# Optimization experiments

Measured on AMD Instinct MI355X. Metric: run time of the kernel, lower is better.

The kernel has to match this reference:

```python
import jax, jax.numpy as jnp
import numpy as np

N_NODES = 100000
C = 128
E = 800000
V = 50000
NEG_SLOPE = 0.2


def gat_conv(x, edges, W, att_src, att_dst, bias, num_nodes):
    """Single-head PyG-style GATConv with self-loops added (PyG default).

    edges: [2, E] with row 0 = source j, row 1 = destination i.
    """
    loops = jnp.arange(num_nodes, dtype=edges.dtype)
    src = jnp.concatenate([edges[0], loops])  # [E+N]
    dst = jnp.concatenate([edges[1], loops])

    h = x @ W.T                               # [N, C] linear transform
    a_s = h @ att_src                         # [N] per-node src score
    a_d = h @ att_dst                         # [N] per-node dst score

    e = jax.nn.leaky_relu(a_s[src] + a_d[dst], NEG_SLOPE)  # [E+N]
    # scatter-softmax over edges grouped by destination node
    m = jax.ops.segment_max(e, dst, num_segments=num_nodes)
    ex = jnp.exp(e - m[dst])
    denom = jax.ops.segment_sum(ex, dst, num_segments=num_nodes)
    alpha = ex / (denom[dst] + 1e-16)         # [E+N]

    out = jax.ops.segment_sum(alpha[:, None] * h[src], dst, num_segments=num_nodes)
    return out + bias


def setup_inputs() -> dict:
    key = jax.random.key(0)
    ks = jax.random.split(key, 12)
    s = 1.0 / np.sqrt(C)
    return {
        "embedding": jax.random.normal(ks[0], (N_NODES, C), jnp.float32),
        "W1": jax.random.normal(ks[1], (C, C), jnp.float32) * s,
        "att_src1": jax.random.normal(ks[2], (C,), jnp.float32) * s,
        "att_dst1": jax.random.normal(ks[3], (C,), jnp.float32) * s,
        "b1": jax.random.normal(ks[4], (C,), jnp.float32) * s,
        "W2": jax.random.normal(ks[5], (C, C), jnp.float32) * s,
        "att_src2": jax.random.normal(ks[6], (C,), jnp.float32) * s,
        "att_dst2": jax.random.normal(ks[7], (C,), jnp.float32) * s,
        "b2": jax.random.normal(ks[8], (C,), jnp.float32) * s,
        "edges1": jax.random.randint(ks[9], (2, E), 0, N_NODES, jnp.int64 if jax.config.jax_enable_x64 else jnp.int32),
        "edges2": jax.random.randint(ks[10], (2, E), 0, N_NODES, jnp.int64 if jax.config.jax_enable_x64 else jnp.int32),
        "idx_mapping": jax.random.randint(ks[11], (V,), 0, N_NODES, jnp.int64 if jax.config.jax_enable_x64 else jnp.int32),
    }


def reference(embedding, W1, att_src1, att_dst1, b1, W2, att_src2, att_dst2, b2,
              edges1, edges2, idx_mapping):
    h = gat_conv(embedding, edges1, W1, att_src1, att_dst1, b1, N_NODES)
    h = gat_conv(h, edges2, W2, att_src2, att_dst2, b2, N_NODES)
    return h[idx_mapping]
```

## Files before the change

kernel.cpp:

```cpp
#include <hip/hip_runtime.h>

#define N_NODES 100000
#define C_DIM 128
#define E_EDGES 800000
#define V_OUT 50000
#define EN (E_EDGES + N_NODES)
#define M2 (2 * N_NODES)
#define EN2 (2 * EN)

#define BSHIFT 8
#define NBUCK_L ((N_NODES + 255) >> 8)
#define NBUCK2 (2 * NBUCK_L)
#define CAP 4096
#define P1_CHUNK 4096
#define P1_PER_T (P1_CHUNK / 256)
#define NCHUNK ((EN2 + P1_CHUNK - 1) / P1_CHUNK)
#define VFLAG_BLKS ((V_OUT + 255) / 256)

#define XPAD 136
#define LDS_E 768

#define GEMM_BLKS ((N_NODES + 63) / 64)

typedef unsigned int uint;
typedef unsigned short ushort;
typedef __attribute__((ext_vector_type(8))) short bf16x8;
typedef __attribute__((ext_vector_type(4))) float f32x4;

static __device__ __forceinline__ ushort f2bf(float f) {
    uint u = __float_as_uint(f);
    u += 0x7fffu + ((u >> 16) & 1);
    return (ushort)(u >> 16);
}

template <int IN_F32>
static __device__ __forceinline__ void gemm_body(
    char* smem, int gb, int tid,
    const void* __restrict__ xin, const float* __restrict__ W,
    const float* __restrict__ att_s, const float* __restrict__ att_d,
    ushort* __restrict__ hb, float* __restrict__ a_s, float* __restrict__ a_d)
{
    ushort* ws = (ushort*)smem;

    {
        const int row = tid >> 1, half = tid & 1;
        const float* src = W + row * 128 + half * 64;
        ushort* dst = &ws[row * XPAD + half * 64];
        #pragma unroll
        for (int i = 0; i < 8; ++i) {
            float4 u = *reinterpret_cast<const float4*>(src + i * 8);
            float4 v = *reinterpret_cast<const float4*>(src + i * 8 + 4);
            uint4 pk;
            pk.x = (uint)f2bf(u.x) | ((uint)f2bf(u.y) << 16);
            pk.y = (uint)f2bf(u.z) | ((uint)f2bf(u.w) << 16);
            pk.z = (uint)f2bf(v.x) | ((uint)f2bf(v.y) << 16);
            pk.w = (uint)f2bf(v.z) | ((uint)f2bf(v.w) << 16);
            *reinterpret_cast<uint4*>(dst + i * 8) = pk;
        }
    }

    const int lane = tid & 63, wv = tid >> 6;
    const int m = lane & 15, quad = lane >> 4;
    const int nb = gb * 64;
    const int n0 = nb + wv * 16;
    const long xrow = min((long)(n0 + m), (long)N_NODES - 1);

    bf16x8 a[4];
    if (IN_F32) {
        const float* src = (const float*)xin + xrow * 128 + quad * 8;
        #pragma unroll
        for (int ki = 0; ki < 4; ++ki) {
            float4 u = *reinterpret_cast<const float4*>(src + ki * 32);
            float4 v = *reinterpret_cast<const float4*>(src + ki * 32 + 4);
            uint4 pk;
            pk.x = (uint)f2bf(u.x) | ((uint)f2bf(u.y) << 16);
            pk.y = (uint)f2bf(u.z) | ((uint)f2bf(u.w) << 16);
            pk.z = (uint)f2bf(v.x) | ((uint)f2bf(v.y) << 16);
            pk.w = (uint)f2bf(v.z) | ((uint)f2bf(v.w) << 16);
            a[ki] = *reinterpret_cast<bf16x8*>(&pk);
        }
    } else {
        const ushort* src = (const ushort*)xin + xrow * 128 + quad * 8;
        #pragma unroll
        for (int ki = 0; ki < 4; ++ki)
            a[ki] = *reinterpret_cast<const bf16x8*>(src + ki * 32);
    }
    __syncthreads();

    float ps[4] = {0, 0, 0, 0}, pd[4] = {0, 0, 0, 0};
    uint2 packed[8];
    #pragma unroll
    for (int ct = 0; ct < 8; ++ct) {
        const int cc = ct * 16 + m;
        f32x4 acc = {0.f, 0.f, 0.f, 0.f};
        #pragma unroll
        for (int ki = 0; ki < 4; ++ki) {
            bf16x8 b = *reinterpret_cast<const bf16x8*>(&ws[cc * XPAD + quad * 8 + ki * 32]);
            acc = __builtin_amdgcn_mfma_f32_16x16x32_bf16(a[ki], b, acc, 0, 0, 0);
        }
        const float asc = att_s[cc], adc = att_d[cc];
        #pragma unroll
        for (int r = 0; r < 4; ++r) {
            ps[r] = fmaf(acc[r], asc, ps[r]);
            pd[r] = fmaf(acc[r], adc, pd[r]);
        }
        packed[ct].x = (uint)f2bf(acc[0]) | ((uint)f2bf(acc[1]) << 16);
        packed[ct].y = (uint)f2bf(acc[2]) | ((uint)f2bf(acc[3]) << 16);
    }
    __syncthreads();

    {
        const int rowb = (wv * 16 + quad * 4) * XPAD + m;
        #pragma unroll
        for (int ct = 0; ct < 8; ++ct) {
            ws[rowb            + ct * 16] = (ushort)(packed[ct].x);
            ws[rowb +     XPAD + ct * 16] = (ushort)(packed[ct].x >> 16);
            ws[rowb + 2 * XPAD + ct * 16] = (ushort)(packed[ct].y);
            ws[rowb + 3 * XPAD + ct * 16] = (ushort)(packed[ct].y >> 16);
        }
    }
    __syncthreads();

    {
        const int sub = tid & 15, rb = tid >> 4;
        #pragma unroll
        for (int i = 0; i < 4; ++i) {
            const int rl = rb + i * 16;
            const int node = nb + rl;
            uint4 v = *reinterpret_cast<const uint4*>(&ws[rl * XPAD + sub * 8]);
            if (node < N_NODES)
                *reinterpret_cast<uint4*>(hb + (long)node * 128 + sub * 8) = v;
        }
    }
    #pragma unroll
    for (int r = 0; r < 4; ++r) {
        float s = ps[r], d = pd[r];
        #pragma unroll
        for (int x = 1; x < 16; x <<= 1) { s += __shfl_xor(s, x); d += __shfl_xor(d, x); }
        const int node = n0 + quad * 4 + r;
        if (m == 0 && node < N_NODES) { a_s[node] = s; a_d[node] = d; }
    }
}

static __device__ __forceinline__ void partition_body(
    char* smem, int pb, int tid,
    const int* __restrict__ e1, const int* __restrict__ e2,
    int* __restrict__ cursor, uint* __restrict__ slab)
{
    int* cnt     = (int*)smem;
    int* basearr = cnt + NBUCK2;
    for (int i = tid; i < NBUCK2; i += 256) cnt[i] = 0;
    __syncthreads();

    const int e0 = pb * P1_CHUNK;
    uint ent[P1_PER_T];
    int  bkt[P1_PER_T];
    #pragma unroll
    for (int i = 0; i < P1_PER_T; ++i) {
        int e = e0 + i * 256 + tid;
        bkt[i] = -1;
        if (e < EN2) {
            int src, dst, lb;
            if (e < EN) {
                if (e < E_EDGES) { src = e1[e]; dst = e1[E_EDGES + e]; }
                else             { src = dst = e - E_EDGES; }
                lb = 0;
            } else {
                int f = e - EN;
                if (f < E_EDGES) { src = e2[f]; dst = e2[E_EDGES + f]; }
                else             { src = dst = f - E_EDGES; }
                lb = NBUCK_L;
            }
            bkt[i] = lb + (dst >> BSHIFT);
            ent[i] = (uint)src | ((uint)(dst & 255) << 17);
            atomicAdd(&cnt[bkt[i]], 1);
        }
    }
    __syncthreads();
    for (int b = tid; b < NBUCK2; b += 256) {
        int c = cnt[b];
        basearr[b] = (c > 0) ? atomicAdd(&cursor[b], c) : 0;
        cnt[b] = 0;
    }
    __syncthreads();
    #pragma unroll
    for (int i = 0; i < P1_PER_T; ++i) {
        if (bkt[i] >= 0) {
            int r = basearr[bkt[i]] + atomicAdd(&cnt[bkt[i]], 1);
            if (r < CAP) slab[(long)bkt[i] * CAP + r] = ent[i];
        }
    }
}

__global__ __launch_bounds__(256, 4) void front_kernel(
    const float* __restrict__ emb, const float* __restrict__ W1,
    const float* __restrict__ as1, const float* __restrict__ ad1,
    ushort* __restrict__ hb, float* __restrict__ aS, float* __restrict__ aD,
    const int* __restrict__ e1, const int* __restrict__ e2,
    int* __restrict__ cursor, uint* __restrict__ slab,
    const int* __restrict__ idxm, int* __restrict__ head, int* __restrict__ nextp)
{
    __shared__ __attribute__((aligned(16))) char smem[128 * XPAD * 2];
    const int b = blockIdx.x;
    const int tid = threadIdx.x;
    if (b < GEMM_BLKS) {
        gemm_body<1>(smem, b, tid, emb, W1, as1, ad1, hb, aS, aD);
    } else if (b < GEMM_BLKS + NCHUNK) {
        partition_body(smem, b - GEMM_BLKS, tid, e1, e2, cursor, slab);
    } else {
        int v = (b - GEMM_BLKS - NCHUNK) * 256 + tid;
        if (v < V_OUT) {
            int n = idxm[v];
            int old = atomicExch(&head[n], v + 1);
            nextp[v] = old;
        }
    }
}

__global__ __launch_bounds__(256, 4) void gemm2_kernel(
    const ushort* __restrict__ a1o, const float* __restrict__ W2,
    const float* __restrict__ as2, const float* __restrict__ ad2,
    ushort* __restrict__ hb, float* __restrict__ aS, float* __restrict__ aD)
{
    __shared__ __attribute__((aligned(16))) char smem[128 * XPAD * 2];
    gemm_body<0>(smem, blockIdx.x, threadIdx.x, a1o, W2, as2, ad2, hb, aS, aD);
}

__global__ __launch_bounds__(256) void local_csr(
    const uint* __restrict__ slab, const int* __restrict__ cursor,
    int* __restrict__ offs, uint* __restrict__ esrc)
{
    __shared__ uint ent[CAP];
    __shared__ int deg[256];
    __shared__ int excl[256];
    __shared__ int sbase;
    const int b = blockIdx.x;
    const int tid = threadIdx.x;
    const int cnt = min(cursor[b], CAP);
    const int layer = (b >= NBUCK_L);
    const int node0 = (b - layer * NBUCK_L) << BSHIFT;
    const int obase = layer * N_NODES;
    const int nodes_n = min(256, N_NODES - node0);

    if (tid < 256) deg[tid & 255] = 0;
    if (tid < 64) {
        int s = 0;
        #pragma unroll
        for (int k = 0; k < 13; ++k) {
            int idx = tid + 64 * k;
            if (idx < b) s += cursor[idx];
        }
        #pragma unroll
        for (int d = 32; d > 0; d >>= 1) s += __shfl_down(s, d);
        if (tid == 0) sbase = s;
    }
    __syncthreads();
    const int base = sbase;

    for (int i = tid; i < cnt; i += 256) {
        uint v = slab[(long)b * CAP + i];
        ent[i] = v;
        atomicAdd(&deg[v >> 17], 1);
    }
    __syncthreads();
    if (tid < 64) {
        int v4[4]; int s = 0;
        #pragma unroll
        for (int i = 0; i < 4; ++i) { v4[i] = deg[tid * 4 + i]; s += v4[i]; }
        int incl = s;
        #pragma unroll
        for (int d = 1; d < 64; d <<= 1) {
            int t = __shfl_up(incl, d);
            if (tid >= d) incl += t;
        }
        int e = incl - s;
        #pragma unroll
        for (int i = 0; i < 4; ++i) { excl[tid * 4 + i] = e; e += v4[i]; }
    }
    __syncthreads();
    for (int i = tid; i < nodes_n; i += 256)
        offs[obase + node0 + i] = base + excl[i];
    if (tid < 256) deg[tid & 255] = 0;
    if (tid == 0 && node0 + 256 >= N_NODES)
        offs[obase + N_NODES] = base + cnt;
    __syncthreads();
    for (int i = tid; i < cnt; i += 256) {
        uint v = ent[i];
        int dl = v >> 17;
        int r = atomicAdd(&deg[dl], 1);
        esrc[base + excl[dl] + r] = v;
    }
}

template <int MODE>
__global__ __launch_bounds__(256) void aggregate(
    const ushort* __restrict__ hb, const float* __restrict__ a_s,
    const float* __restrict__ a_d, const float* __restrict__ bias,
    const int* __restrict__ offs, const uint* __restrict__ esrc,
    const int* __restrict__ head, const int* __restrict__ nextp,
    void* __restrict__ outp, int obase)
{
    __shared__ uint2 ew[LDS_E];
    const int tid = threadIdx.x;
    const int node0 = blockIdx.x * 16;
    const int bnode0 = (node0 >> BSHIFT) << BSHIFT;
    const int bstart = offs[obase + node0];
    const int bend   = offs[obase + node0 + 16];
    const int nE = bend - bstart;

    for (int i = tid; i < min(nE, LDS_E); i += 256) {
        uint v = esrc[bstart + i];
        float w = 0.0f;
        const int d = bnode0 + (v >> 17);
        if (MODE == 0 || head[d] != 0) {
            float e = a_s[v & 0x1ffff] + a_d[d];
            e = (e >= 0.0f) ? e : 0.2f * e;
            w = __expf(e);
        }
        ew[i] = make_uint2(v, __float_as_uint(w));
    }
    __syncthreads();

    const int wave = tid >> 6;
    const int lane = tid & 63;
    const int slot = lane >> 4;
    const int c16  = lane & 15;
    const int node = node0 + wave * 4 + slot;
    int hv = 0;
    if (MODE == 1) {
        hv = head[node];
        if (hv == 0) return;
    }

    const int start = offs[obase + node];
    const int end   = offs[obase + node + 1];
    const long coff = (long)(c16 << 3);
    float acc[8] = {0, 0, 0, 0, 0, 0, 0, 0};
    float dsum = 0.0f;

    if (start < end) {
        if (nE <= LDS_E) {
            const int jr = start - bstart, jend = end - bstart;
            const int e1 = jend - 1;
            uint2 p0 = ew[jr];
            uint2 p1 = ew[min(jr + 1, e1)];
            uint2 p2 = ew[min(jr + 2, e1)];
            uint2 p3 = ew[min(jr + 3, e1)];
            uint4 h0 = *reinterpret_cast<const uint4*>(hb + ((long)(p0.x & 0x1ffff) << 7) + coff);
            uint4 h1 = *reinterpret_cast<const uint4*>(hb + ((long)(p1.x & 0x1ffff) << 7) + coff);
            uint4 h2 = *reinterpret_cast<const uint4*>(hb + ((long)(p2.x & 0x1ffff) << 7) + coff);
            uint4 h3 = *reinterpret_cast<const uint4*>(hb + ((long)(p3.x & 0x1ffff) << 7) + coff);
            float w0 = __uint_as_float(p0.y);
            float w1 = __uint_as_float(p1.y);
            float w2 = __uint_as_float(p2.y);
            float w3 = __uint_as_float(p3.y);
            for (int j = jr; j < jend; ++j) {
                uint2 p4 = ew[min(j + 4, e1)];
                uint4 h4 = *reinterpret_cast<const uint4*>(hb + ((long)(p4.x & 0x1ffff) << 7) + coff);
                float w4 = __uint_as_float(p4.y);
                dsum += w0;
                acc[0] = fmaf(w0, __uint_as_float(h0.x << 16),         acc[0]);
                acc[1] = fmaf(w0, __uint_as_float(h0.x & 0xffff0000u), acc[1]);
                acc[2] = fmaf(w0, __uint_as_float(h0.y << 16),         acc[2]);
                acc[3] = fmaf(w0, __uint_as_float(h0.y & 0xffff0000u), acc[3]);
                acc[4] = fmaf(w0, __uint_as_float(h0.z << 16),         acc[4]);
                acc[5] = fmaf(w0, __uint_as_float(h0.z & 0xffff0000u), acc[5]);
                acc[6] = fmaf(w0, __uint_as_float(h0.w << 16),         acc[6]);
                acc[7] = fmaf(w0, __uint_as_float(h0.w & 0xffff0000u), acc[7]);
                w0 = w1; w1 = w2; w2 = w3; w3 = w4;
                h0 = h1; h1 = h2; h2 = h3; h3 = h4;
            }
        } else {
            const float ad = a_d[node];
            for (int j = start; j < end; ++j) {
                uint v = esrc[j];
                float e = a_s[v & 0x1ffff] + ad;
                e = (e >= 0.0f) ? e : 0.2f * e;
                float w = __expf(e);
                uint4 h = *reinterpret_cast<const uint4*>(hb + ((long)(v & 0x1ffff) << 7) + coff);
                dsum += w;
                acc[0] = fmaf(w, __uint_as_float(h.x << 16),         acc[0]);
                acc[1] = fmaf(w, __uint_as_float(h.x & 0xffff0000u), acc[1]);
                acc[2] = fmaf(w, __uint_as_float(h.y << 16),         acc[2]);
                acc[3] = fmaf(w, __uint_as_float(h.y & 0xffff0000u), acc[3]);
                acc[4] = fmaf(w, __uint_as_float(h.z << 16),         acc[4]);
                acc[5] = fmaf(w, __uint_as_float(h.z & 0xffff0000u), acc[5]);
                acc[6] = fmaf(w, __uint_as_float(h.w << 16),         acc[6]);
                acc[7] = fmaf(w, __uint_as_float(h.w & 0xffff0000u), acc[7]);
            }
        }
    }

    const float inv = 1.0f / (dsum + 1e-16f);
    const int c0 = c16 << 3;
    const float4 b0 = *reinterpret_cast<const float4*>(bias + c0);
    const float4 b1 = *reinterpret_cast<const float4*>(bias + c0 + 4);
    float res[8];
    res[0] = fmaf(acc[0], inv, b0.x);
    res[1] = fmaf(acc[1], inv, b0.y);
    res[2] = fmaf(acc[2], inv, b0.z);
    res[3] = fmaf(acc[3], inv, b0.w);
    res[4] = fmaf(acc[4], inv, b1.x);
    res[5] = fmaf(acc[5], inv, b1.y);
    res[6] = fmaf(acc[6], inv, b1.z);
    res[7] = fmaf(acc[7], inv, b1.w);
    if (MODE == 0) {
        uint4 pk;
        pk.x = (uint)f2bf(res[0]) | ((uint)f2bf(res[1]) << 16);
        pk.y = (uint)f2bf(res[2]) | ((uint)f2bf(res[3]) << 16);
        pk.z = (uint)f2bf(res[4]) | ((uint)f2bf(res[5]) << 16);
        pk.w = (uint)f2bf(res[6]) | ((uint)f2bf(res[7]) << 16);
        *reinterpret_cast<uint4*>((ushort*)outp + ((long)node << 7) + c0) = pk;
    } else {
        const float4 r0 = make_float4(res[0], res[1], res[2], res[3]);
        const float4 r1 = make_float4(res[4], res[5], res[6], res[7]);
        for (int v1 = hv; v1 != 0; v1 = nextp[v1 - 1]) {
            float* op = (float*)outp + ((long)(v1 - 1) << 7) + c0;
            *reinterpret_cast<float4*>(op)     = r0;
            *reinterpret_cast<float4*>(op + 4) = r1;
        }
    }
}

extern "C" void kernel_launch(void* const* d_in, const int* in_sizes, int n_in,
                              void* d_out, int out_size, void* d_ws, size_t ws_size,
                              hipStream_t stream)
{
    const float* emb = (const float*)d_in[0];
    const float* W1  = (const float*)d_in[1];
    const float* as1 = (const float*)d_in[2];
    const float* ad1 = (const float*)d_in[3];
    const float* b1  = (const float*)d_in[4];
    const float* W2  = (const float*)d_in[5];
    const float* as2 = (const float*)d_in[6];
    const float* ad2 = (const float*)d_in[7];
    const float* b2  = (const float*)d_in[8];
    const int* edges1 = (const int*)d_in[9];
    const int* edges2 = (const int*)d_in[10];
    const int* idxm   = (const int*)d_in[11];
    float* out = (float*)d_out;

    char* p = (char*)d_ws;
    auto alloc = [&](size_t bytes) {
        char* r = p;
        p += (bytes + 255) & ~(size_t)255;
        return r;
    };
    ushort* hb   = (ushort*)alloc((size_t)N_NODES * C_DIM * 2);
    ushort* a1o  = (ushort*)alloc((size_t)N_NODES * C_DIM * 2);
    uint*   slab = (uint*)alloc((size_t)NBUCK2 * CAP * 4);
    uint*   esrc = (uint*)alloc((size_t)EN2 * 4);
    int*    offs = (int*)alloc((size_t)(M2 + 1) * 4);
    float*  aS   = (float*)alloc((size_t)N_NODES * 4);
    float*  aD   = (float*)alloc((size_t)N_NODES * 4);
    int*  nextp  = (int*)alloc((size_t)V_OUT * 4);
    int*  cursor = (int*)alloc((size_t)NBUCK2 * 4);
    int*  head   = (int*)alloc((size_t)N_NODES * 4);

    hipMemsetAsync(cursor, 0,
                   (size_t)((char*)head - (char*)cursor) + (size_t)N_NODES * 4, stream);

    front_kernel<<<GEMM_BLKS + NCHUNK + VFLAG_BLKS, 256, 0, stream>>>(
        emb, W1, as1, ad1, hb, aS, aD, edges1, edges2, cursor, slab,
        idxm, head, nextp);

    local_csr<<<NBUCK2, 256, 0, stream>>>(slab, cursor, offs, esrc);

    aggregate<0><<<N_NODES / 16, 256, 0, stream>>>(hb, aS, aD, b1, offs, esrc, head, nextp, a1o, 0);

    gemm2_kernel<<<GEMM_BLKS, 256, 0, stream>>>(a1o, W2, as2, ad2, hb, aS, aD);
    aggregate<1><<<N_NODES / 16, 256, 0, stream>>>(hb, aS, aD, b2, offs, esrc, head, nextp, out, N_NODES);
}
```

Before: 259.2 us.

## Build CSR via global degree count and atomic scatter instead of bucket slabs

Replaces the two-stage bucket partition (slab with fixed capacity, then per-bucket local CSR in LDS) with a per-node global degree histogram, a per-bucket offset scan, and a separate scatter kernel that places each edge using a global atomic decrement. This removes the slab buffer and its CAP overflow limit, and the local LDS sort. In exchange it adds global atomics per edge twice, rereads the edge arrays in a new kernel, adds a launch, and makes the within-node edge order nondeterministic.

```diff
diff --git a/kernel.cpp b/kernel.cpp
--- a/kernel.cpp
+++ b/kernel.cpp
@@ -11,11 +11,13 @@
 #define BSHIFT 8
 #define NBUCK_L ((N_NODES + 255) >> 8)
 #define NBUCK2 (2 * NBUCK_L)
-#define CAP 4096
 #define P1_CHUNK 4096
 #define P1_PER_T (P1_CHUNK / 256)
 #define NCHUNK ((EN2 + P1_CHUNK - 1) / P1_CHUNK)
 #define VFLAG_BLKS ((V_OUT + 255) / 256)
+#define SC_CHUNK 1024
+#define SC_PER_T (SC_CHUNK / 256)
+#define NSCHUNK ((EN2 + SC_CHUNK - 1) / SC_CHUNK)
 
 #define XPAD 136
 #define LDS_E 768
@@ -31,6 +33,22 @@
     uint u = __float_as_uint(f);
     u += 0x7fffu + ((u >> 16) & 1);
     return (ushort)(u >> 16);
+}
+
+static __device__ __forceinline__ void edge_decode(
+    int e, const int* __restrict__ e1, const int* __restrict__ e2,
+    int& src, int& dst, int& layer)
+{
+    if (e < EN) {
+        if (e < E_EDGES) { src = e1[e]; dst = e1[E_EDGES + e]; }
+        else             { src = dst = e - E_EDGES; }
+        layer = 0;
+    } else {
+        int f = e - EN;
+        if (f < E_EDGES) { src = e2[f]; dst = e2[E_EDGES + f]; }
+        else             { src = dst = f - E_EDGES; }
+        layer = 1;
+    }
 }
 
 template <int IN_F32>
@@ -142,53 +160,30 @@
     }
 }
 
-static __device__ __forceinline__ void partition_body(
+static __device__ __forceinline__ void deg_body(
     char* smem, int pb, int tid,
     const int* __restrict__ e1, const int* __restrict__ e2,
-    int* __restrict__ cursor, uint* __restrict__ slab)
-{
-    int* cnt     = (int*)smem;
-    int* basearr = cnt + NBUCK2;
+    int* __restrict__ deg, int* __restrict__ bucketTot)
+{
+    int* cnt = (int*)smem;
     for (int i = tid; i < NBUCK2; i += 256) cnt[i] = 0;
     __syncthreads();
 
     const int e0 = pb * P1_CHUNK;
-    uint ent[P1_PER_T];
-    int  bkt[P1_PER_T];
     #pragma unroll
     for (int i = 0; i < P1_PER_T; ++i) {
         int e = e0 + i * 256 + tid;
-        bkt[i] = -1;
         if (e < EN2) {
-            int src, dst, lb;
-            if (e < EN) {
-                if (e < E_EDGES) { src = e1[e]; dst = e1[E_EDGES + e]; }
-                else             { src = dst = e - E_EDGES; }
-                lb = 0;
-            } else {
-                int f = e - EN;
-                if (f < E_EDGES) { src = e2[f]; dst = e2[E_EDGES + f]; }
-                else             { src = dst = f - E_EDGES; }
-                lb = NBUCK_L;
-            }
-            bkt[i] = lb + (dst >> BSHIFT);
-            ent[i] = (uint)src | ((uint)(dst & 255) << 17);
-            atomicAdd(&cnt[bkt[i]], 1);
+            int src, dst, layer;
+            edge_decode(e, e1, e2, src, dst, layer);
+            atomicAdd(&deg[layer * N_NODES + dst], 1);
+            atomicAdd(&cnt[layer * NBUCK_L + (dst >> BSHIFT)], 1);
         }
     }
     __syncthreads();
     for (int b = tid; b < NBUCK2; b += 256) {
         int c = cnt[b];
-        basearr[b] = (c > 0) ? atomicAdd(&cursor[b], c) : 0;
-        cnt[b] = 0;
-    }
-    __syncthreads();
-    #pragma unroll
-    for (int i = 0; i < P1_PER_T; ++i) {
-        if (bkt[i] >= 0) {
-            int r = basearr[bkt[i]] + atomicAdd(&cnt[bkt[i]], 1);
-            if (r < CAP) slab[(long)bkt[i] * CAP + r] = ent[i];
-        }
+        if (c > 0) atomicAdd(&bucketTot[b], c);
     }
 }
 
@@ -197,7 +192,7 @@
     const float* __restrict__ as1, const float* __restrict__ ad1,
     ushort* __restrict__ hb, float* __restrict__ aS, float* __restrict__ aD,
     const int* __restrict__ e1, const int* __restrict__ e2,
-    int* __restrict__ cursor, uint* __restrict__ slab,
+    int* __restrict__ deg, int* __restrict__ bucketTot,
     const int* __restrict__ idxm, int* __restrict__ head, int* __restrict__ nextp)
 {
     __shared__ __attribute__((aligned(16))) char smem[128 * XPAD * 2];
@@ -206,7 +201,7 @@
     if (b < GEMM_BLKS) {
         gemm_body<1>(smem, b, tid, emb, W1, as1, ad1, hb, aS, aD);
     } else if (b < GEMM_BLKS + NCHUNK) {
-        partition_body(smem, b - GEMM_BLKS, tid, e1, e2, cursor, slab);
+        deg_body(smem, b - GEMM_BLKS, tid, e1, e2, deg, bucketTot);
     } else {
         int v = (b - GEMM_BLKS - NCHUNK) * 256 + tid;
         if (v < V_OUT) {
@@ -226,47 +221,37 @@
     gemm_body<0>(smem, blockIdx.x, threadIdx.x, a1o, W2, as2, ad2, hb, aS, aD);
 }
 
-__global__ __launch_bounds__(256) void local_csr(
-    const uint* __restrict__ slab, const int* __restrict__ cursor,
-    int* __restrict__ offs, uint* __restrict__ esrc)
-{
-    __shared__ uint ent[CAP];
-    __shared__ int deg[256];
+__global__ __launch_bounds__(256) void offs_kernel(
+    const int* __restrict__ deg, const int* __restrict__ bucketTot,
+    int* __restrict__ offs)
+{
+    __shared__ int degl[256];
     __shared__ int excl[256];
     __shared__ int sbase;
     const int b = blockIdx.x;
     const int tid = threadIdx.x;
-    const int cnt = min(cursor[b], CAP);
     const int layer = (b >= NBUCK_L);
     const int node0 = (b - layer * NBUCK_L) << BSHIFT;
     const int obase = layer * N_NODES;
     const int nodes_n = min(256, N_NODES - node0);
 
-    if (tid < 256) deg[tid & 255] = 0;
+    degl[tid] = (tid < nodes_n) ? deg[obase + node0 + tid] : 0;
     if (tid < 64) {
         int s = 0;
         #pragma unroll
         for (int k = 0; k < 13; ++k) {
             int idx = tid + 64 * k;
-            if (idx < b) s += cursor[idx];
+            if (idx < b) s += bucketTot[idx];
         }
         #pragma unroll
         for (int d = 32; d > 0; d >>= 1) s += __shfl_down(s, d);
         if (tid == 0) sbase = s;
     }
     __syncthreads();
-    const int base = sbase;
-
-    for (int i = tid; i < cnt; i += 256) {
-        uint v = slab[(long)b * CAP + i];
-        ent[i] = v;
-        atomicAdd(&deg[v >> 17], 1);
-    }
-    __syncthreads();
     if (tid < 64) {
         int v4[4]; int s = 0;
         #pragma unroll
-        for (int i = 0; i < 4; ++i) { v4[i] = deg[tid * 4 + i]; s += v4[i]; }
+        for (int i = 0; i < 4; ++i) { v4[i] = degl[tid * 4 + i]; s += v4[i]; }
         int incl = s;
         #pragma unroll
         for (int d = 1; d < 64; d <<= 1) {
@@ -278,17 +263,27 @@
         for (int i = 0; i < 4; ++i) { excl[tid * 4 + i] = e; e += v4[i]; }
     }
     __syncthreads();
-    for (int i = tid; i < nodes_n; i += 256)
-        offs[obase + node0 + i] = base + excl[i];
-    if (tid < 256) deg[tid & 255] = 0;
-    if (tid == 0 && node0 + 256 >= N_NODES)
-        offs[obase + N_NODES] = base + cnt;
-    __syncthreads();
-    for (int i = tid; i < cnt; i += 256) {
-        uint v = ent[i];
-        int dl = v >> 17;
-        int r = atomicAdd(&deg[dl], 1);
-        esrc[base + excl[dl] + r] = v;
+    if (tid < nodes_n) offs[obase + node0 + tid] = sbase + excl[tid];
+    if (b == NBUCK2 - 1 && tid == 0) offs[M2] = EN2;
+}
+
+__global__ __launch_bounds__(256) void scatter_kernel(
+    const int* __restrict__ e1, const int* __restrict__ e2,
+    const int* __restrict__ offs, int* __restrict__ deg,
+    uint* __restrict__ esrc)
+{
+    const int tid = threadIdx.x;
+    const int e0 = blockIdx.x * SC_CHUNK;
+    #pragma unroll
+    for (int i = 0; i < SC_PER_T; ++i) {
+        int e = e0 + i * 256 + tid;
+        if (e < EN2) {
+            int src, dst, layer;
+            edge_decode(e, e1, e2, src, dst, layer);
+            const int k = layer * N_NODES + dst;
+            int ret = atomicAdd(&deg[k], -1);
+            esrc[offs[k] + ret - 1] = (uint)src | ((uint)(dst & 255) << 17);
+        }
     }
 }
 
@@ -448,23 +443,24 @@
     };
     ushort* hb   = (ushort*)alloc((size_t)N_NODES * C_DIM * 2);
     ushort* a1o  = (ushort*)alloc((size_t)N_NODES * C_DIM * 2);
-    uint*   slab = (uint*)alloc((size_t)NBUCK2 * CAP * 4);
     uint*   esrc = (uint*)alloc((size_t)EN2 * 4);
     int*    offs = (int*)alloc((size_t)(M2 + 1) * 4);
     float*  aS   = (float*)alloc((size_t)N_NODES * 4);
     float*  aD   = (float*)alloc((size_t)N_NODES * 4);
     int*  nextp  = (int*)alloc((size_t)V_OUT * 4);
-    int*  cursor = (int*)alloc((size_t)NBUCK2 * 4);
-    int*  head   = (int*)alloc((size_t)N_NODES * 4);
-
-    hipMemsetAsync(cursor, 0,
-                   (size_t)((char*)head - (char*)cursor) + (size_t)N_NODES * 4, stream);
+    int*  deg       = (int*)alloc((size_t)M2 * 4);
+    int*  bucketTot = (int*)alloc((size_t)NBUCK2 * 4);
+    int*  head      = (int*)alloc((size_t)N_NODES * 4);
+
+    hipMemsetAsync(deg, 0,
+                   (size_t)((char*)head - (char*)deg) + (size_t)N_NODES * 4, stream);
 
     front_kernel<<<GEMM_BLKS + NCHUNK + VFLAG_BLKS, 256, 0, stream>>>(
-        emb, W1, as1, ad1, hb, aS, aD, edges1, edges2, cursor, slab,
+        emb, W1, as1, ad1, hb, aS, aD, edges1, edges2, deg, bucketTot,
         idxm, head, nextp);
 
-    local_csr<<<NBUCK2, 256, 0, stream>>>(slab, cursor, offs, esrc);
+    offs_kernel<<<NBUCK2, 256, 0, stream>>>(deg, bucketTot, offs);
+    scatter_kernel<<<NSCHUNK, 256, 0, stream>>>(edges1, edges2, offs, deg, esrc);
 
     aggregate<0><<<N_NODES / 16, 256, 0, stream>>>(hb, aS, aD, b1, offs, esrc, head, nextp, a1o, 0);
 
```

Measured after the change: 382.6 us. +47.6%, slower.

## Fuse all stages into one persistent cooperative kernel with grid syncs

Applied to the files above, without the earlier changes.

Replaces the memset plus five kernel launches with a single cooperative persistent kernel. It loops blocks over the work units of each stage and separates the stages with grid.sync, keeping a multi-kernel fallback path. The weights are pre-converted to bf16 once and read straight from global memory in the GEMM instead of being staged into LDS per block, which shrinks shared memory to about 17 KB (CAP lowered to 3584) so more blocks can be resident. The aim is to remove launch overheads and per-block weight conversion, at the cost of grid-wide barriers, fixed grid sizing, and B-operand loads from global/L2.

```diff
diff --git a/kernel.cpp b/kernel.cpp
--- a/kernel.cpp
+++ b/kernel.cpp
@@ -1,4 +1,5 @@
 #include <hip/hip_runtime.h>
+#include <hip/hip_cooperative_groups.h>
 
 #define N_NODES 100000
 #define C_DIM 128
@@ -11,7 +12,7 @@
 #define BSHIFT 8
 #define NBUCK_L ((N_NODES + 255) >> 8)
 #define NBUCK2 (2 * NBUCK_L)
-#define CAP 4096
+#define CAP 3584
 #define P1_CHUNK 4096
 #define P1_PER_T (P1_CHUNK / 256)
 #define NCHUNK ((EN2 + P1_CHUNK - 1) / P1_CHUNK)
@@ -21,6 +22,11 @@
 #define LDS_E 768
 
 #define GEMM_BLKS ((N_NODES + 63) / 64)
+#define AGG_BLKS (N_NODES / 16)
+#define P1_UNITS (GEMM_BLKS + NCHUNK + VFLAG_BLKS)
+#define NCU 256
+
+#define SMEM_BYTES 17408
 
 typedef unsigned int uint;
 typedef unsigned short ushort;
@@ -36,29 +42,11 @@
 template <int IN_F32>
 static __device__ __forceinline__ void gemm_body(
     char* smem, int gb, int tid,
-    const void* __restrict__ xin, const float* __restrict__ W,
+    const void* __restrict__ xin, const ushort* __restrict__ Wb,
     const float* __restrict__ att_s, const float* __restrict__ att_d,
     ushort* __restrict__ hb, float* __restrict__ a_s, float* __restrict__ a_d)
 {
-    ushort* ws = (ushort*)smem;
-
-    {
-        const int row = tid >> 1, half = tid & 1;
-        const float* src = W + row * 128 + half * 64;
-        ushort* dst = &ws[row * XPAD + half * 64];
-        #pragma unroll
-        for (int i = 0; i < 8; ++i) {
-            float4 u = *reinterpret_cast<const float4*>(src + i * 8);
-            float4 v = *reinterpret_cast<const float4*>(src + i * 8 + 4);
-            uint4 pk;
-            pk.x = (uint)f2bf(u.x) | ((uint)f2bf(u.y) << 16);
-            pk.y = (uint)f2bf(u.z) | ((uint)f2bf(u.w) << 16);
-            pk.z = (uint)f2bf(v.x) | ((uint)f2bf(v.y) << 16);
-            pk.w = (uint)f2bf(v.z) | ((uint)f2bf(v.w) << 16);
-            *reinterpret_cast<uint4*>(dst + i * 8) = pk;
-        }
-    }
-
+    ushort* xs = (ushort*)smem;
     const int lane = tid & 63, wv = tid >> 6;
     const int m = lane & 15, quad = lane >> 4;
     const int nb = gb * 64;
@@ -85,7 +73,6 @@
         for (int ki = 0; ki < 4; ++ki)
             a[ki] = *reinterpret_cast<const bf16x8*>(src + ki * 32);
     }
-    __syncthreads();
 
     float ps[4] = {0, 0, 0, 0}, pd[4] = {0, 0, 0, 0};
     uint2 packed[8];
@@ -95,7 +82,7 @@
         f32x4 acc = {0.f, 0.f, 0.f, 0.f};
         #pragma unroll
         for (int ki = 0; ki < 4; ++ki) {
-            bf16x8 b = *reinterpret_cast<const bf16x8*>(&ws[cc * XPAD + quad * 8 + ki * 32]);
+            bf16x8 b = *reinterpret_cast<const bf16x8*>(Wb + cc * 128 + quad * 8 + ki * 32);
             acc = __builtin_amdgcn_mfma_f32_16x16x32_bf16(a[ki], b, acc, 0, 0, 0);
         }
         const float asc = att_s[cc], adc = att_d[cc];
@@ -107,16 +94,15 @@
         packed[ct].x = (uint)f2bf(acc[0]) | ((uint)f2bf(acc[1]) << 16);
         packed[ct].y = (uint)f2bf(acc[2]) | ((uint)f2bf(acc[3]) << 16);
     }
-    __syncthreads();
 
     {
         const int rowb = (wv * 16 + quad * 4) * XPAD + m;
         #pragma unroll
         for (int ct = 0; ct < 8; ++ct) {
-            ws[rowb            + ct * 16] = (ushort)(packed[ct].x);
-            ws[rowb +     XPAD + ct * 16] = (ushort)(packed[ct].x >> 16);
-            ws[rowb + 2 * XPAD + ct * 16] = (ushort)(packed[ct].y);
-            ws[rowb + 3 * XPAD + ct * 16] = (ushort)(packed[ct].y >> 16);
+            xs[rowb            + ct * 16] = (ushort)(packed[ct].x);
+            xs[rowb +     XPAD + ct * 16] = (ushort)(packed[ct].x >> 16);
+            xs[rowb + 2 * XPAD + ct * 16] = (ushort)(packed[ct].y);
+            xs[rowb + 3 * XPAD + ct * 16] = (ushort)(packed[ct].y >> 16);
         }
     }
     __syncthreads();
@@ -127,7 +113,7 @@
         for (int i = 0; i < 4; ++i) {
             const int rl = rb + i * 16;
             const int node = nb + rl;
-            uint4 v = *reinterpret_cast<const uint4*>(&ws[rl * XPAD + sub * 8]);
+            uint4 v = *reinterpret_cast<const uint4*>(&xs[rl * XPAD + sub * 8]);
             if (node < N_NODES)
                 *reinterpret_cast<uint4*>(hb + (long)node * 128 + sub * 8) = v;
         }
@@ -192,19 +178,290 @@
     }
 }
 
+static __device__ __forceinline__ void local_csr_body(
+    char* smem, int b, int tid,
+    const uint* __restrict__ slab, const int* __restrict__ cursor,
+    int* __restrict__ offs, uint* __restrict__ esrc)
+{
+    uint* ent   = (uint*)smem;
+    int*  deg   = (int*)(smem + CAP * 4);
+    int*  excl  = deg + 256;
+    int*  sbase = excl + 256;
+    const int cnt = min(cursor[b], CAP);
+    const int layer = (b >= NBUCK_L);
+    const int node0 = (b - layer * NBUCK_L) << BSHIFT;
+    const int obase = layer * N_NODES;
+    const int nodes_n = min(256, N_NODES - node0);
+
+    deg[tid] = 0;
+    if (tid < 64) {
+        int s = 0;
+        #pragma unroll
+        for (int k = 0; k < 13; ++k) {
+            int idx = tid + 64 * k;
+            if (idx < b) s += cursor[idx];
+        }
+        #pragma unroll
+        for (int d = 32; d > 0; d >>= 1) s += __shfl_down(s, d);
+        if (tid == 0) *sbase = s;
+    }
+    __syncthreads();
+    const int base = *sbase;
+
+    for (int i = tid; i < cnt; i += 256) {
+        uint v = slab[(long)b * CAP + i];
+        ent[i] = v;
+        atomicAdd(&deg[v >> 17], 1);
+    }
+    __syncthreads();
+    if (tid < 64) {
+        int v4[4]; int s = 0;
+        #pragma unroll
+        for (int i = 0; i < 4; ++i) { v4[i] = deg[tid * 4 + i]; s += v4[i]; }
+        int incl = s;
+        #pragma unroll
+        for (int d = 1; d < 64; d <<= 1) {
+            int t = __shfl_up(incl, d);
+            if (tid >= d) incl += t;
+        }
+        int e = incl - s;
+        #pragma unroll
+        for (int i = 0; i < 4; ++i) { excl[tid * 4 + i] = e; e += v4[i]; }
+    }
+    __syncthreads();
+    if (tid < nodes_n) offs[obase + node0 + tid] = base + excl[tid];
+    deg[tid] = 0;
+    if (tid == 0 && node0 + 256 >= N_NODES)
+        offs[obase + N_NODES] = base + cnt;
+    __syncthreads();
+    for (int i = tid; i < cnt; i += 256) {
+        uint v = ent[i];
+        int dl = v >> 17;
+        int r = atomicAdd(&deg[dl], 1);
+        esrc[base + excl[dl] + r] = v;
+    }
+}
+
+template <int MODE>
+static __device__ __forceinline__ void aggregate_body(
+    char* smem, int blk, int tid,
+    const ushort* __restrict__ hb, const float* __restrict__ a_s,
+    const float* __restrict__ a_d, const float* __restrict__ bias,
+    const int* __restrict__ offs, const uint* __restrict__ esrc,
+    const int* __restrict__ head, const int* __restrict__ nextp,
+    void* __restrict__ outp, int obase)
+{
+    uint2* ew = (uint2*)smem;
+    const int node0 = blk * 16;
+    const int bnode0 = (node0 >> BSHIFT) << BSHIFT;
+    const int bstart = offs[obase + node0];
+    const int bend   = offs[obase + node0 + 16];
+    const int nE = bend - bstart;
+
+    for (int i = tid; i < min(nE, LDS_E); i += 256) {
+        uint v = esrc[bstart + i];
+        float w = 0.0f;
+        const int d = bnode0 + (v >> 17);
+        if (MODE == 0 || head[d] != 0) {
+            float e = a_s[v & 0x1ffff] + a_d[d];
+            e = (e >= 0.0f) ? e : 0.2f * e;
+            w = __expf(e);
+        }
+        ew[i] = make_uint2(v, __float_as_uint(w));
+    }
+    __syncthreads();
+
+    const int wave = tid >> 6;
+    const int lane = tid & 63;
+    const int slot = lane >> 4;
+    const int c16  = lane & 15;
+    const int node = node0 + wave * 4 + slot;
+    int hv = 0;
+    bool active = true;
+    if (MODE == 1) {
+        hv = head[node];
+        active = (hv != 0);
+    }
+
+    if (active) {
+        const int start = offs[obase + node];
+        const int end   = offs[obase + node + 1];
+        const long coff = (long)(c16 << 3);
+        float acc[8] = {0, 0, 0, 0, 0, 0, 0, 0};
+        float dsum = 0.0f;
+
+        if (start < end) {
+            if (nE <= LDS_E) {
+                const int jr = start - bstart, jend = end - bstart;
+                const int e1 = jend - 1;
+                uint2 p0 = ew[jr];
+                uint2 p1 = ew[min(jr + 1, e1)];
+                uint2 p2 = ew[min(jr + 2, e1)];
+                uint2 p3 = ew[min(jr + 3, e1)];
+                uint4 h0 = *reinterpret_cast<const uint4*>(hb + ((long)(p0.x & 0x1ffff) << 7) + coff);
+                uint4 h1 = *reinterpret_cast<const uint4*>(hb + ((long)(p1.x & 0x1ffff) << 7) + coff);
+                uint4 h2 = *reinterpret_cast<const uint4*>(hb + ((long)(p2.x & 0x1ffff) << 7) + coff);
+                uint4 h3 = *reinterpret_cast<const uint4*>(hb + ((long)(p3.x & 0x1ffff) << 7) + coff);
+                float w0 = __uint_as_float(p0.y);
+                float w1 = __uint_as_float(p1.y);
+                float w2 = __uint_as_float(p2.y);
+                float w3 = __uint_as_float(p3.y);
+                for (int j = jr; j < jend; ++j) {
+                    uint2 p4 = ew[min(j + 4, e1)];
+                    uint4 h4 = *reinterpret_cast<const uint4*>(hb + ((long)(p4.x & 0x1ffff) << 7) + coff);
+                    float w4 = __uint_as_float(p4.y);
+                    dsum += w0;
+                    acc[0] = fmaf(w0, __uint_as_float(h0.x << 16),         acc[0]);
+                    acc[1] = fmaf(w0, __uint_as_float(h0.x & 0xffff0000u), acc[1]);
+                    acc[2] = fmaf(w0, __uint_as_float(h0.y << 16),         acc[2]);
+                    acc[3] = fmaf(w0, __uint_as_float(h0.y & 0xffff0000u), acc[3]);
+                    acc[4] = fmaf(w0, __uint_as_float(h0.z << 16),         acc[4]);
+                    acc[5] = fmaf(w0, __uint_as_float(h0.z & 0xffff0000u), acc[5]);
+                    acc[6] = fmaf(w0, __uint_as_float(h0.w << 16),         acc[6]);
+                    acc[7] = fmaf(w0, __uint_as_float(h0.w & 0xffff0000u), acc[7]);
+                    w0 = w1; w1 = w2; w2 = w3; w3 = w4;
+                    h0 = h1; h1 = h2; h2 = h3; h3 = h4;
+                }
+            } else {
+                const float ad = a_d[node];
+                for (int j = start; j < end; ++j) {
+                    uint v = esrc[j];
+                    float e = a_s[v & 0x1ffff] + ad;
+                    e = (e >= 0.0f) ? e : 0.2f * e;
+                    float w = __expf(e);
+                    uint4 h = *reinterpret_cast<const uint4*>(hb + ((long)(v & 0x1ffff) << 7) + coff);
+                    dsum += w;
+                    acc[0] = fmaf(w, __uint_as_float(h.x << 16),         acc[0]);
+                    acc[1] = fmaf(w, __uint_as_float(h.x & 0xffff0000u), acc[1]);
+                    acc[2] = fmaf(w, __uint_as_float(h.y << 16),         acc[2]);
+                    acc[3] = fmaf(w, __uint_as_float(h.y & 0xffff0000u), acc[3]);
+                    acc[4] = fmaf(w, __uint_as_float(h.z << 16),         acc[4]);
+                    acc[5] = fmaf(w, __uint_as_float(h.z & 0xffff0000u), acc[5]);
+                    acc[6] = fmaf(w, __uint_as_float(h.w << 16),         acc[6]);
+                    acc[7] = fmaf(w, __uint_as_float(h.w & 0xffff0000u), acc[7]);
+                }
+            }
+        }
+
+        const float inv = 1.0f / (dsum + 1e-16f);
+        const int c0 = c16 << 3;
+        const float4 b0 = *reinterpret_cast<const float4*>(bias + c0);
+        const float4 b1 = *reinterpret_cast<const float4*>(bias + c0 + 4);
+        float res[8];
+        res[0] = fmaf(acc[0], inv, b0.x);
+        res[1] = fmaf(acc[1], inv, b0.y);
+        res[2] = fmaf(acc[2], inv, b0.z);
+        res[3] = fmaf(acc[3], inv, b0.w);
+        res[4] = fmaf(acc[4], inv, b1.x);
+        res[5] = fmaf(acc[5], inv, b1.y);
+        res[6] = fmaf(acc[6], inv, b1.z);
+        res[7] = fmaf(acc[7], inv, b1.w);
+        if (MODE == 0) {
+            uint4 pk;
+            pk.x = (uint)f2bf(res[0]) | ((uint)f2bf(res[1]) << 16);
+            pk.y = (uint)f2bf(res[2]) | ((uint)f2bf(res[3]) << 16);
+            pk.z = (uint)f2bf(res[4]) | ((uint)f2bf(res[5]) << 16);
+            pk.w = (uint)f2bf(res[6]) | ((uint)f2bf(res[7]) << 16);
+            *reinterpret_cast<uint4*>((ushort*)outp + ((long)node << 7) + c0) = pk;
+        } else {
+            const float4 r0 = make_float4(res[0], res[1], res[2], res[3]);
+            const float4 r1 = make_float4(res[4], res[5], res[6], res[7]);
+            for (int v1 = hv; v1 != 0; v1 = nextp[v1 - 1]) {
+                float* op = (float*)outp + ((long)(v1 - 1) << 7) + c0;
+                *reinterpret_cast<float4*>(op)     = r0;
+                *reinterpret_cast<float4*>(op + 4) = r1;
+            }
+        }
+    }
+}
+
+__global__ __launch_bounds__(256, 4) void mega_kernel(
+    const float* emb, const float* W1, const float* as1, const float* ad1, const float* b1,
+    const float* W2, const float* as2, const float* ad2, const float* b2,
+    const int* e1, const int* e2, const int* idxm, float* out,
+    ushort* hb, ushort* a1o, uint* slab, uint* esrc, int* offs,
+    float* aS, float* aD, int* nextp, int* cursor, int* head,
+    ushort* W1b, ushort* W2b)
+{
+    __shared__ __attribute__((aligned(16))) char smem[SMEM_BYTES];
+    cooperative_groups::grid_group grid = cooperative_groups::this_grid();
+    const int tid = threadIdx.x;
+    const int bid = blockIdx.x;
+    const int nb  = gridDim.x;
+    const int gt  = bid * 256 + tid, gs = nb * 256;
+
+    for (int i = gt; i < C_DIM * C_DIM; i += gs) {
+        W1b[i] = f2bf(W1[i]);
+        W2b[i] = f2bf(W2[i]);
+    }
+    for (int i = gt; i < NBUCK2; i += gs) cursor[i] = 0;
+    for (int i = gt; i < N_NODES; i += gs) head[i] = 0;
+    grid.sync();
+
+    for (int u = bid; u < P1_UNITS; u += nb) {
+        if (u < GEMM_BLKS) {
+            gemm_body<1>(smem, u, tid, emb, W1b, as1, ad1, hb, aS, aD);
+        } else if (u < GEMM_BLKS + NCHUNK) {
+            partition_body(smem, u - GEMM_BLKS, tid, e1, e2, cursor, slab);
+        } else {
+            int v = (u - GEMM_BLKS - NCHUNK) * 256 + tid;
+            if (v < V_OUT) {
+                int n = idxm[v];
+                int old = atomicExch(&head[n], v + 1);
+                nextp[v] = old;
+            }
+        }
+        __syncthreads();
+    }
+    grid.sync();
+
+    for (int u = bid; u < NBUCK2; u += nb) {
+        local_csr_body(smem, u, tid, slab, cursor, offs, esrc);
+        __syncthreads();
+    }
+    grid.sync();
+
+    for (int u = bid; u < AGG_BLKS; u += nb) {
+        aggregate_body<0>(smem, u, tid, hb, aS, aD, b1, offs, esrc, head, nextp, a1o, 0);
+        __syncthreads();
+    }
+    grid.sync();
+
+    for (int u = bid; u < GEMM_BLKS; u += nb) {
+        gemm_body<0>(smem, u, tid, a1o, W2b, as2, ad2, hb, aS, aD);
+        __syncthreads();
+    }
+    grid.sync();
+
+    for (int u = bid; u < AGG_BLKS; u += nb) {
+        aggregate_body<1>(smem, u, tid, hb, aS, aD, b2, offs, esrc, head, nextp, out, N_NODES);
+        __syncthreads();
+    }
+}
+
+__global__ void prep_kernel(const float* __restrict__ W1, const float* __restrict__ W2,
+                            ushort* __restrict__ W1b, ushort* __restrict__ W2b)
+{
+    int i = blockIdx.x * 256 + threadIdx.x;
+    if (i < C_DIM * C_DIM) {
+        W1b[i] = f2bf(W1[i]);
+        W2b[i] = f2bf(W2[i]);
+    }
+}
+
 __global__ __launch_bounds__(256, 4) void front_kernel(
-    const float* __restrict__ emb, const float* __restrict__ W1,
+    const float* __restrict__ emb, const ushort* __restrict__ W1b,
     const float* __restrict__ as1, const float* __restrict__ ad1,
     ushort* __restrict__ hb, float* __restrict__ aS, float* __restrict__ aD,
     const int* __restrict__ e1, const int* __restrict__ e2,
     int* __restrict__ cursor, uint* __restrict__ slab,
     const int* __restrict__ idxm, int* __restrict__ head, int* __restrict__ nextp)
 {
-    __shared__ __attribute__((aligned(16))) char smem[128 * XPAD * 2];
+    __shared__ __attribute__((aligned(16))) char smem[SMEM_BYTES];
     const int b = blockIdx.x;
     const int tid = threadIdx.x;
     if (b < GEMM_BLKS) {
-        gemm_body<1>(smem, b, tid, emb, W1, as1, ad1, hb, aS, aD);
+        gemm_body<1>(smem, b, tid, emb, W1b, as1, ad1, hb, aS, aD);
     } else if (b < GEMM_BLKS + NCHUNK) {
         partition_body(smem, b - GEMM_BLKS, tid, e1, e2, cursor, slab);
     } else {
@@ -217,209 +474,34 @@
     }
 }
 
-__global__ __launch_bounds__(256, 4) void gemm2_kernel(
-    const ushort* __restrict__ a1o, const float* __restrict__ W2,
-    const float* __restrict__ as2, const float* __restrict__ ad2,
-    ushort* __restrict__ hb, float* __restrict__ aS, float* __restrict__ aD)
-{
-    __shared__ __attribute__((aligned(16))) char smem[128 * XPAD * 2];
-    gemm_body<0>(smem, blockIdx.x, threadIdx.x, a1o, W2, as2, ad2, hb, aS, aD);
-}
-
-__global__ __launch_bounds__(256) void local_csr(
+__global__ __launch_bounds__(256) void csr_kernel(
     const uint* __restrict__ slab, const int* __restrict__ cursor,
     int* __restrict__ offs, uint* __restrict__ esrc)
 {
-    __shared__ uint ent[CAP];
-    __shared__ int deg[256];
-    __shared__ int excl[256];
-    __shared__ int sbase;
-    const int b = blockIdx.x;
-    const int tid = threadIdx.x;
-    const int cnt = min(cursor[b], CAP);
-    const int layer = (b >= NBUCK_L);
-    const int node0 = (b - layer * NBUCK_L) << BSHIFT;
-    const int obase = layer * N_NODES;
-    const int nodes_n = min(256, N_NODES - node0);
-
-    if (tid < 256) deg[tid & 255] = 0;
-    if (tid < 64) {
-        int s = 0;
-        #pragma unroll
-        for (int k = 0; k < 13; ++k) {
-            int idx = tid + 64 * k;
-            if (idx < b) s += cursor[idx];
-        }
-        #pragma unroll
-        for (int d = 32; d > 0; d >>= 1) s += __shfl_down(s, d);
-        if (tid == 0) sbase = s;
-    }
-    __syncthreads();
-    const int base = sbase;
-
-    for (int i = tid; i < cnt; i += 256) {
-        uint v = slab[(long)b * CAP + i];
-        ent[i] = v;
-        atomicAdd(&deg[v >> 17], 1);
-    }
-    __syncthreads();
-    if (tid < 64) {
-        int v4[4]; int s = 0;
-        #pragma unroll
-        for (int i = 0; i < 4; ++i) { v4[i] = deg[tid * 4 + i]; s += v4[i]; }
-        int incl = s;
-        #pragma unroll
-        for (int d = 1; d < 64; d <<= 1) {
-            int t = __shfl_up(incl, d);
-            if (tid >= d) incl += t;
-        }
-        int e = incl - s;
-        #pragma unroll
-        for (int i = 0; i < 4; ++i) { excl[tid * 4 + i] = e; e += v4[i]; }
-    }
-    __syncthreads();
-    for (int i = tid; i < nodes_n; i += 256)
-        offs[obase + node0 + i] = base + excl[i];
-    if (tid < 256) deg[tid & 255] = 0;
-    if (tid == 0 && node0 + 256 >= N_NODES)
-        offs[obase + N_NODES] = base + cnt;
-    __syncthreads();
-    for (int i = tid; i < cnt; i += 256) {
-        uint v = ent[i];
-        int dl = v >> 17;
-        int r = atomicAdd(&deg[dl], 1);
-        esrc[base + excl[dl] + r] = v;
-    }
+    __shared__ __attribute__((aligned(16))) char smem[SMEM_BYTES];
+    local_csr_body(smem, blockIdx.x, threadIdx.x, slab, cursor, offs, esrc);
 }
 
 template <int MODE>
-__global__ __launch_bounds__(256) void aggregate(
+__global__ __launch_bounds__(256) void agg_kernel(
     const ushort* __restrict__ hb, const float* __restrict__ a_s,
     const float* __restrict__ a_d, const float* __restrict__ bias,
     const int* __restrict__ offs, const uint* __restrict__ esrc,
     const int* __restrict__ head, const int* __restrict__ nextp,
     void* __restrict__ outp, int obase)
 {
-    __shared__ uint2 ew[LDS_E];
-    const int tid = threadIdx.x;
-    const int node0 = blockIdx.x * 16;
-    const int bnode0 = (node0 >> BSHIFT) << BSHIFT;
-    const int bstart = offs[obase + node0];
-    const int bend   = offs[obase + node0 + 16];
-    const int nE = bend - bstart;
-
-    for (int i = tid; i < min(nE, LDS_E); i += 256) {
-        uint v = esrc[bstart + i];
-        float w = 0.0f;
-        const int d = bnode0 + (v >> 17);
-        if (MODE == 0 || head[d] != 0) {
-            float e = a_s[v & 0x1ffff] + a_d[d];
-            e = (e >= 0.0f) ? e : 0.2f * e;
-            w = __expf(e);
-        }
-        ew[i] = make_uint2(v, __float_as_uint(w));
-    }
-    __syncthreads();
-
-    const int wave = tid >> 6;
-    const int lane = tid & 63;
-    const int slot = lane >> 4;
-    const int c16  = lane & 15;
-    const int node = node0 + wave * 4 + slot;
-    int hv = 0;
-    if (MODE == 1) {
-        hv = head[node];
-        if (hv == 0) return;
-    }
-
-    const int start = offs[obase + node];
-    const int end   = offs[obase + node + 1];
-    const long coff = (long)(c16 << 3);
-    float acc[8] = {0, 0, 0, 0, 0, 0, 0, 0};
-    float dsum = 0.0f;
-
-    if (start < end) {
-        if (nE <= LDS_E) {
-            const int jr = start - bstart, jend = end - bstart;
-            const int e1 = jend - 1;
-            uint2 p0 = ew[jr];
-            uint2 p1 = ew[min(jr + 1, e1)];
-            uint2 p2 = ew[min(jr + 2, e1)];
-            uint2 p3 = ew[min(jr + 3, e1)];
-            uint4 h0 = *reinterpret_cast<const uint4*>(hb + ((long)(p0.x & 0x1ffff) << 7) + coff);
-            uint4 h1 = *reinterpret_cast<const uint4*>(hb + ((long)(p1.x & 0x1ffff) << 7) + coff);
-            uint4 h2 = *reinterpret_cast<const uint4*>(hb + ((long)(p2.x & 0x1ffff) << 7) + coff);
-            uint4 h3 = *reinterpret_cast<const uint4*>(hb + ((long)(p3.x & 0x1ffff) << 7) + coff);
-            float w0 = __uint_as_float(p0.y);
-            float w1 = __uint_as_float(p1.y);
-            float w2 = __uint_as_float(p2.y);
-            float w3 = __uint_as_float(p3.y);
-            for (int j = jr; j < jend; ++j) {
-                uint2 p4 = ew[min(j + 4, e1)];
-                uint4 h4 = *reinterpret_cast<const uint4*>(hb + ((long)(p4.x & 0x1ffff) << 7) + coff);
-                float w4 = __uint_as_float(p4.y);
-                dsum += w0;
-                acc[0] = fmaf(w0, __uint_as_float(h0.x << 16),         acc[0]);
-                acc[1] = fmaf(w0, __uint_as_float(h0.x & 0xffff0000u), acc[1]);
-                acc[2] = fmaf(w0, __uint_as_float(h0.y << 16),         acc[2]);
-                acc[3] = fmaf(w0, __uint_as_float(h0.y & 0xffff0000u), acc[3]);
-                acc[4] = fmaf(w0, __uint_as_float(h0.z << 16),         acc[4]);
-                acc[5] = fmaf(w0, __uint_as_float(h0.z & 0xffff0000u), acc[5]);
-                acc[6] = fmaf(w0, __uint_as_float(h0.w << 16),         acc[6]);
-                acc[7] = fmaf(w0, __uint_as_float(h0.w & 0xffff0000u), acc[7]);
-                w0 = w1; w1 = w2; w2 = w3; w3 = w4;
-                h0 = h1; h1 = h2; h2 = h3; h3 = h4;
-            }
-        } else {
-            const float ad = a_d[node];
-            for (int j = start; j < end; ++j) {
-                uint v = esrc[j];
-                float e = a_s[v & 0x1ffff] + ad;
-                e = (e >= 0.0f) ? e : 0.2f * e;
-                float w = __expf(e);
-                uint4 h = *reinterpret_cast<const uint4*>(hb + ((long)(v & 0x1ffff) << 7) + coff);
-                dsum += w;
-                acc[0] = fmaf(w, __uint_as_float(h.x << 16),         acc[0]);
-                acc[1] = fmaf(w, __uint_as_float(h.x & 0xffff0000u), acc[1]);
-                acc[2] = fmaf(w, __uint_as_float(h.y << 16),         acc[2]);
-                acc[3] = fmaf(w, __uint_as_float(h.y & 0xffff0000u), acc[3]);
-                acc[4] = fmaf(w, __uint_as_float(h.z << 16),         acc[4]);
-                acc[5] = fmaf(w, __uint_as_float(h.z & 0xffff0000u), acc[5]);
-                acc[6] = fmaf(w, __uint_as_float(h.w << 16),         acc[6]);
-                acc[7] = fmaf(w, __uint_as_float(h.w & 0xffff0000u), acc[7]);
-            }
-        }
-    }
-
-    const float inv = 1.0f / (dsum + 1e-16f);
-    const int c0 = c16 << 3;
-    const float4 b0 = *reinterpret_cast<const float4*>(bias + c0);
-    const float4 b1 = *reinterpret_cast<const float4*>(bias + c0 + 4);
-    float res[8];
-    res[0] = fmaf(acc[0], inv, b0.x);
-    res[1] = fmaf(acc[1], inv, b0.y);
-    res[2] = fmaf(acc[2], inv, b0.z);
-    res[3] = fmaf(acc[3], inv, b0.w);
-    res[4] = fmaf(acc[4], inv, b1.x);
-    res[5] = fmaf(acc[5], inv, b1.y);
-    res[6] = fmaf(acc[6], inv, b1.z);
-    res[7] = fmaf(acc[7], inv, b1.w);
-    if (MODE == 0) {
-        uint4 pk;
-        pk.x = (uint)f2bf(res[0]) | ((uint)f2bf(res[1]) << 16);
-        pk.y = (uint)f2bf(res[2]) | ((uint)f2bf(res[3]) << 16);
-        pk.z = (uint)f2bf(res[4]) | ((uint)f2bf(res[5]) << 16);
-        pk.w = (uint)f2bf(res[6]) | ((uint)f2bf(res[7]) << 16);
-        *reinterpret_cast<uint4*>((ushort*)outp + ((long)node << 7) + c0) = pk;
-    } else {
-        const float4 r0 = make_float4(res[0], res[1], res[2], res[3]);
-        const float4 r1 = make_float4(res[4], res[5], res[6], res[7]);
-        for (int v1 = hv; v1 != 0; v1 = nextp[v1 - 1]) {
-            float* op = (float*)outp + ((long)(v1 - 1) << 7) + c0;
-            *reinterpret_cast<float4*>(op)     = r0;
-            *reinterpret_cast<float4*>(op + 4) = r1;
-        }
-    }
+    __shared__ __attribute__((aligned(16))) char smem[LDS_E * 8];
+    aggregate_body<MODE>(smem, blockIdx.x, threadIdx.x, hb, a_s, a_d, bias,
+                         offs, esrc, head, nextp, outp, obase);
+}
+
+__global__ __launch_bounds__(256, 4) void gemm2_kernel(
+    const ushort* __restrict__ a1o, const ushort* __restrict__ W2b,
+    const float* __restrict__ as2, const float* __restrict__ ad2,
+    ushort* __restrict__ hb, float* __restrict__ aS, float* __restrict__ aD)
+{
+    __shared__ __attribute__((aligned(16))) char smem[SMEM_BYTES];
+    gemm_body<0>(smem, blockIdx.x, threadIdx.x, a1o, W2b, as2, ad2, hb, aS, aD);
 }
 
 extern "C" void kernel_launch(void* const* d_in, const int* in_sizes, int n_in,
@@ -454,20 +536,39 @@
     float*  aS   = (float*)alloc((size_t)N_NODES * 4);
     float*  aD   = (float*)alloc((size_t)N_NODES * 4);
     int*  nextp  = (int*)alloc((size_t)V_OUT * 4);
+    ushort* W1b  = (ushort*)alloc((size_t)C_DIM * C_DIM * 2);
+    ushort* W2b  = (ushort*)alloc((size_t)C_DIM * C_DIM * 2);
     int*  cursor = (int*)alloc((size_t)NBUCK2 * 4);
     int*  head   = (int*)alloc((size_t)N_NODES * 4);
 
-    hipMemsetAsync(cursor, 0,
-                   (size_t)((char*)head - (char*)cursor) + (size_t)N_NODES * 4, stream);
-
-    front_kernel<<<GEMM_BLKS + NCHUNK + VFLAG_BLKS, 256, 0, stream>>>(
-        emb, W1, as1, ad1, hb, aS, aD, edges1, edges2, cursor, slab,
-        idxm, head, nextp);
-
-    local_csr<<<NBUCK2, 256, 0, stream>>>(slab, cursor, offs, esrc);
-
-    aggregate<0><<<N_NODES / 16, 256, 0, stream>>>(hb, aS, aD, b1, offs, esrc, head, nextp, a1o, 0);
-
-    gemm2_kernel<<<GEMM_BLKS, 256, 0, stream>>>(a1o, W2, as2, ad2, hb, aS, aD);
-    aggregate<1><<<N_NODES / 16, 256, 0, stream>>>(hb, aS, aD, b2, offs, esrc, head, nextp, out, N_NODES);
-}
+    int occ = 0;
+    hipError_t qe = hipOccupancyMaxActiveBlocksPerMultiprocessor(
+        &occ, (const void*)mega_kernel, 256, 0);
+    bool launched = false;
+    if (qe == hipSuccess && occ >= 4) {
+        int grid = (occ > 8 ? 8 : occ) * NCU;
+        void* kargs[] = {
+            (void*)&emb, (void*)&W1, (void*)&as1, (void*)&ad1, (void*)&b1,
+            (void*)&W2, (void*)&as2, (void*)&ad2, (void*)&b2,
+            (void*)&edges1, (void*)&edges2, (void*)&idxm, (void*)&out,
+            (void*)&hb, (void*)&a1o, (void*)&slab, (void*)&esrc, (void*)&offs,
+            (void*)&aS, (void*)&aD, (void*)&nextp, (void*)&cursor, (void*)&head,
+            (void*)&W1b, (void*)&W2b
+        };
+        launched = (hipLaunchCooperativeKernel((const void*)mega_kernel, dim3(grid),
+                                               dim3(256), kargs, 0, stream) == hipSuccess);
+    }
+
+    if (!launched) {
+        hipMemsetAsync(cursor, 0,
+                       (size_t)((char*)head - (char*)cursor) + (size_t)N_NODES * 4, stream);
+        prep_kernel<<<(C_DIM * C_DIM + 255) / 256, 256, 0, stream>>>(W1, W2, W1b, W2b);
+        front_kernel<<<P1_UNITS, 256, 0, stream>>>(
+            emb, W1b, as1, ad1, hb, aS, aD, edges1, edges2, cursor, slab,
+            idxm, head, nextp);
+        csr_kernel<<<NBUCK2, 256, 0, stream>>>(slab, cursor, offs, esrc);
+        agg_kernel<0><<<AGG_BLKS, 256, 0, stream>>>(hb, aS, aD, b1, offs, esrc, head, nextp, a1o, 0);
+        gemm2_kernel<<<GEMM_BLKS, 256, 0, stream>>>(a1o, W2b, as2, ad2, hb, aS, aD);
+        agg_kernel<1><<<AGG_BLKS, 256, 0, stream>>>(hb, aS, aD, b2, offs, esrc, head, nextp, out, N_NODES);
+    }
+}
```

Result: slower. 280.2 us (+8.1%).
